# Performance work log

Measured on AMD Instinct MI355X. Metric: run time of the kernel, lower is better.

## Reference

```python
import jax, jax.numpy as jnp
import numpy as np

N_HEADS = 8
D_MODEL = 256
HEAD_DEPTH = D_MODEL // N_HEADS
B, S = 2, 4096


def setup_inputs() -> dict:
    key = jax.random.key(0)
    ks = jax.random.split(key, 8)
    scale = 1.0 / np.sqrt(D_MODEL)
    return {
        "q": jax.random.normal(ks[0], (B, S, D_MODEL), dtype=jnp.float32),
        "k": jax.random.normal(ks[1], (B, S, D_MODEL), dtype=jnp.float32),
        "v": jax.random.normal(ks[2], (B, S, D_MODEL), dtype=jnp.float32),
        "mask": jax.random.randint(ks[3], (B, S, S), 0, 2).astype(jnp.bool_),
        "wq": jax.random.normal(ks[4], (D_MODEL, D_MODEL), dtype=jnp.float32) * scale,
        "wk": jax.random.normal(ks[5], (D_MODEL, D_MODEL), dtype=jnp.float32) * scale,
        "wv": jax.random.normal(ks[6], (D_MODEL, D_MODEL), dtype=jnp.float32) * scale,
        "w_out": jax.random.normal(ks[7], (D_MODEL, D_MODEL), dtype=jnp.float32) * scale,
    }


def _split_heads(x):
    # [B, S, D] -> [B, H, S, Dh]
    b, s, _ = x.shape
    return x.reshape(b, s, N_HEADS, HEAD_DEPTH).transpose(0, 2, 1, 3)


def reference(q, k, v, mask, wq, wk, wv, w_out):
    Q = _split_heads(q @ wq)
    K = _split_heads(k @ wk)
    V = _split_heads(v @ wv)
    # [B, H, Sq, Sk]
    scores = jnp.einsum('bhqd,bhkd->bhqk', Q, K) / jnp.sqrt(
        jnp.asarray(HEAD_DEPTH, dtype=Q.dtype))
    # mask True -> -inf, broadcast over heads
    scores = jnp.where(mask[:, None, :, :], -jnp.inf, scores)
    probs = jax.nn.softmax(scores, axis=-1)
    attn = jnp.einsum('bhqk,bhkd->bhqd', probs, V)
    attn = attn.transpose(0, 2, 1, 3).reshape(q.shape[0], -1, D_MODEL)
    return attn @ w_out
```

## Files before the change

kernel.cpp:

```cpp
#include <hip/hip_runtime.h>
#include <stdint.h>

typedef __bf16 bf16;
typedef __bf16 bf16x8 __attribute__((ext_vector_type(8)));
typedef __bf16 bf16x4 __attribute__((ext_vector_type(4)));
typedef float  f32x4  __attribute__((ext_vector_type(4)));
typedef float  f32x8  __attribute__((ext_vector_type(8)));
typedef float  f32x16 __attribute__((ext_vector_type(16)));
typedef float  float4v __attribute__((ext_vector_type(4)));
typedef int    int4v   __attribute__((ext_vector_type(4)));
typedef unsigned int uint;
typedef unsigned long long ull;

#define QSCALE 0.25505003984214403f


__global__ __launch_bounds__(256) void transpose_w(
    const float* __restrict__ w0, const float* __restrict__ w1,
    const float* __restrict__ w2, const float* __restrict__ w3,
    bf16* __restrict__ WT) {
  const int wsel = blockIdx.z;
  const float* W = wsel == 0 ? w0 : wsel == 1 ? w1 : wsel == 2 ? w2 : w3;
  const int k0 = blockIdx.x * 64, n0 = blockIdx.y * 64;
  __shared__ __align__(16) bf16 t[64][72];
  const int tid = threadIdx.x;
  {
    const int kk = (tid >> 4) << 2;
    const int nn = (tid & 15) << 2;
#pragma unroll
    for (int r = 0; r < 4; ++r) {
      float4v a = *(const float4v*)(W + (size_t)(k0 + kk + r) * 256 + n0 + nn);
#pragma unroll
      for (int j = 0; j < 4; ++j) t[nn + j][kk + r] = (bf16)a[j];
    }
  }
  __syncthreads();
  {
    const int ni = tid >> 2;
    const int c  = (tid & 3) * 16;
    bf16x8 o0 = *(const bf16x8*)(&t[ni][c]);
    bf16x8 o1 = *(const bf16x8*)(&t[ni][c + 8]);
    bf16* dst = WT + (size_t)wsel * 65536 + (size_t)(n0 + ni) * 256 + k0 + c;
    *(bf16x8*)dst = o0;
    *(bf16x8*)(dst + 8) = o1;
  }
}

__global__ __launch_bounds__(256) void proj_pack(
    const float* __restrict__ xq, const float* __restrict__ xk, const float* __restrict__ xv,
    const bf16* __restrict__ WT,
    bf16* __restrict__ Qp, bf16* __restrict__ Kp, bf16* __restrict__ Vp,
    const int* __restrict__ mask, uint* __restrict__ M2) {
  __shared__ __align__(16) unsigned char smem[18432];
  const int tid = threadIdx.x;

  if (blockIdx.x >= 768) {
    uint* trans = (uint*)smem;
    const int pid = blockIdx.x - 768;
    const int bb = pid >> 8;
    const int qt = (pid >> 2) & 63, kc = pid & 3;
    const int q0 = qt * 64;
    const int w = tid >> 6, l = tid & 63;
    const int qrow = q0 + w * 16 + (l >> 2);
    const size_t rowbase = ((size_t)(bb * 4096 + qrow)) * 4096 + kc * 1024;
#pragma unroll
    for (int p = 0; p < 8; ++p) {
      const int kdw = p * 4 + (l & 3);
      const int4v* mp = (const int4v*)(mask + rowbase + kdw * 32);
      uint bits = 0;
#pragma unroll
      for (int j = 0; j < 8; ++j) {
        int4v m = mp[j];
#pragma unroll
        for (int i = 0; i < 4; ++i) bits |= (m[i] != 0 ? 1u : 0u) << (j * 4 + i);
      }
      trans[kdw * 72 + w * 16 + (l >> 2)] = bits;
    }
    __syncthreads();
    {
      const int r = tid >> 3, c = (tid & 7) * 4;
      int4v a = *(const int4v*)(trans + r * 72 + c);
      int4v d = *(const int4v*)(trans + r * 72 + c + 32);
      uint* o = M2 + ((size_t)(bb * 128 + kc * 32 + r)) * 4096 + q0;
      *(int4v*)(o + c) = a;
      *(int4v*)(o + c + 32) = d;
    }
    return;
  }

  const int z = blockIdx.x >> 8;
  const int r8 = blockIdx.x & 255;
  const int m0 = (r8 >> 1) * 64, n0 = (r8 & 1) * 128;
  const float* X = z == 0 ? xq : (z == 1 ? xk : xv);
  const bf16* wt = WT + (size_t)z * 65536;
  const int wave = tid >> 6, lane = tid & 63;
  const int nl = lane & 15, quad = lane >> 4;
  const int arow = m0 + wave * 16 + nl;
  const float* xrow = X + (size_t)arow * 256;

  f32x4 zero4 = {0.f, 0.f, 0.f, 0.f};
  f32x4 acc[8];
#pragma unroll
  for (int i = 0; i < 8; ++i) acc[i] = zero4;

  for (int ks = 0; ks < 8; ++ks) {
    float4v a0 = *(const float4v*)(xrow + ks * 32 + quad * 8);
    float4v a1 = *(const float4v*)(xrow + ks * 32 + quad * 8 + 4);
    bf16x8 af;
#pragma unroll
    for (int i = 0; i < 4; ++i) { af[i] = (bf16)a0[i]; af[4 + i] = (bf16)a1[i]; }
#pragma unroll
    for (int nf = 0; nf < 8; ++nf) {
      bf16x8 bfr = *(const bf16x8*)(wt + (size_t)(n0 + nf * 16 + nl) * 256 + ks * 32 + quad * 8);
      acc[nf] = __builtin_amdgcn_mfma_f32_16x16x32_bf16(af, bfr, acc[nf], 0, 0, 0);
    }
  }

  const int bq = m0 >> 12;
  const int s0 = m0 & 4095;
  const int posl = wave * 16 + quad * 4;

  if (z == 2) {
    bf16* tv = (bf16*)smem;
#pragma unroll
    for (int nf = 0; nf < 8; ++nf) {
      const int col = nf * 16 + nl;
      bf16x4 o;
#pragma unroll
      for (int rr = 0; rr < 4; ++rr) o[rr] = (bf16)acc[nf][rr];
      *(bf16x4*)(tv + (size_t)col * 72 + posl) = o;
    }
    __syncthreads();
    const int h2 = tid >> 6, ln = tid & 63;
    const int d = ln & 31, shalf = ln >> 5;
    const int h = (n0 >> 5) + h2;
    bf16* vb = Vp + (size_t)(bq * 8 + h) * 131072 + (size_t)(s0 >> 5) * 1024 + d * 8;
#pragma unroll
    for (int it = 0; it < 4; ++it) {
      const int blk = it >> 1, sub = (it & 1) * 2 + shalf;
      const int K0 = (sub >> 1) * 16 + (sub & 1) * 4;
      const bf16* src = tv + (size_t)(h2 * 32 + d) * 72 + blk * 32 + K0;
      bf16x4 g0 = *(const bf16x4*)(src);
      bf16x4 g1 = *(const bf16x4*)(src + 8);
      bf16x8 o;
#pragma unroll
      for (int j = 0; j < 4; ++j) { o[j] = g0[j]; o[4 + j] = g1[j]; }
      *(bf16x8*)(vb + (size_t)blk * 1024 + sub * 256) = o;
    }
  } else {
    bf16* tq = (bf16*)smem;
    const float scale = (z == 0) ? QSCALE : 1.0f;
#pragma unroll
    for (int nf = 0; nf < 8; ++nf) {
      const int col = nf * 16 + nl;
#pragma unroll
      for (int rr = 0; rr < 4; ++rr)
        tq[(size_t)(posl + rr) * 136 + col] = (bf16)(acc[nf][rr] * scale);
    }
    __syncthreads();
    bf16* Out = z == 0 ? Qp : Kp;
    const int h2 = tid >> 6, ln = tid & 63;
    const int h = (n0 >> 5) + h2;
    const int s = s0 + ln;
    bf16* ob = Out + (size_t)(bq * 8 + h) * 131072 + (size_t)(s >> 5) * 1024 + (s & 31) * 8;
#pragma unroll
    for (int sub = 0; sub < 4; ++sub) {
      bf16x8 o = *(const bf16x8*)(tq + (size_t)ln * 136 + h2 * 32 + sub * 8);
      *(bf16x8*)(ob + sub * 256) = o;
    }
  }
}

__global__ __launch_bounds__(256) void attn_kernel(
    const bf16* __restrict__ Qp, const bf16* __restrict__ Kp,
    const bf16* __restrict__ Vp, const uint* __restrict__ M2,
    bf16* __restrict__ Og) {
  const int id = blockIdx.x;
  const int xcd = id & 7, slot = id >> 3;
  const int bh = xcd * 2 + (slot >> 6);
  const int q0 = (slot & 63) * 64;
  const int b = bh >> 3, h = bh & 7;
  const int tid = threadIdx.x, w = tid >> 6, lane = tid & 63;
  const int nl = lane & 31, half = lane >> 5;

  __shared__ float Ored[4][32][66];
  __shared__ float Lsum[64][8];

  const size_t bhbase = (size_t)bh * 131072;
  const int so0 = half * 256 + nl * 8;
  const int so1 = 512 + half * 256 + nl * 8;

  bf16x8 qf[2][2];
#pragma unroll
  for (int qt = 0; qt < 2; ++qt) {
    const bf16* qb = Qp + bhbase + (size_t)((q0 >> 5) + qt) * 1024;
    qf[qt][0] = *(const bf16x8*)(qb + so0);
    qf[qt][1] = *(const bf16x8*)(qb + so1);
  }

  const bf16* Kw = Kp + bhbase + (size_t)w * 1024;
  const bf16* Vw = Vp + bhbase + (size_t)w * 1024;
  const uint* Mw = M2 + (size_t)b * 524288 + (size_t)w * 4096 + q0 + nl;

  f32x16 z16;
#pragma unroll
  for (int i = 0; i < 16; ++i) z16[i] = 0.f;
  f32x16 acc0 = z16, acc1 = z16;
  float lsum0 = 0.f, lsum1 = 0.f;

  struct Frag { bf16x8 ka0, ka1, va0, va1; uint m0, m1; };
  auto LOADF = [&](int kt) -> Frag {
    Frag f;
    const bf16* kc = Kw + (size_t)kt * 4096;
    const bf16* vc = Vw + (size_t)kt * 4096;
    f.ka0 = *(const bf16x8*)(kc + so0);
    f.ka1 = *(const bf16x8*)(kc + so1);
    f.va0 = *(const bf16x8*)(vc + so0);
    f.va1 = *(const bf16x8*)(vc + so1);
    const uint* mp = Mw + (size_t)kt * 16384;
    f.m0 = mp[0];
    f.m1 = mp[32];
    return f;
  };

  auto STEP = [&](const Frag& f) {
    const int minv0 = (int)((~f.m0) >> (4 * half));
    const int minv1 = (int)((~f.m1) >> (4 * half));
    f32x16 st0 = __builtin_amdgcn_mfma_f32_32x32x16_bf16(f.ka0, qf[0][0], z16, 0, 0, 0);
    st0 = __builtin_amdgcn_mfma_f32_32x32x16_bf16(f.ka1, qf[0][1], st0, 0, 0, 0);
    f32x16 st1 = __builtin_amdgcn_mfma_f32_32x32x16_bf16(f.ka0, qf[1][0], z16, 0, 0, 0);
    st1 = __builtin_amdgcn_mfma_f32_32x32x16_bf16(f.ka1, qf[1][1], st1, 0, 0, 0);

    f32x16 pf0, pf1;
#pragma unroll
    for (int g = 0; g < 4; ++g)
#pragma unroll
      for (int r = 0; r < 4; ++r) {
        const int i = g * 4 + r, off = r + 8 * g;
        float e0 = __builtin_amdgcn_exp2f(st0[i]);
        float e1 = __builtin_amdgcn_exp2f(st1[i]);
        const uint k0m = (uint)__builtin_amdgcn_sbfe(minv0, off, 1);
        const uint k1m = (uint)__builtin_amdgcn_sbfe(minv1, off, 1);
        e0 = __uint_as_float(__float_as_uint(e0) & k0m);
        e1 = __uint_as_float(__float_as_uint(e1) & k1m);
        lsum0 += e0; lsum1 += e1;
        pf0[i] = e0; pf1[i] = e1;
      }
    const bf16x8 pb00 = __builtin_convertvector(
        __builtin_shufflevector(pf0, pf0, 0, 1, 2, 3, 4, 5, 6, 7), bf16x8);
    const bf16x8 pb01 = __builtin_convertvector(
        __builtin_shufflevector(pf0, pf0, 8, 9, 10, 11, 12, 13, 14, 15), bf16x8);
    const bf16x8 pb10 = __builtin_convertvector(
        __builtin_shufflevector(pf1, pf1, 0, 1, 2, 3, 4, 5, 6, 7), bf16x8);
    const bf16x8 pb11 = __builtin_convertvector(
        __builtin_shufflevector(pf1, pf1, 8, 9, 10, 11, 12, 13, 14, 15), bf16x8);

    acc0 = __builtin_amdgcn_mfma_f32_32x32x16_bf16(f.va0, pb00, acc0, 0, 0, 0);
    acc0 = __builtin_amdgcn_mfma_f32_32x32x16_bf16(f.va1, pb01, acc0, 0, 0, 0);
    acc1 = __builtin_amdgcn_mfma_f32_32x32x16_bf16(f.va0, pb10, acc1, 0, 0, 0);
    acc1 = __builtin_amdgcn_mfma_f32_32x32x16_bf16(f.va1, pb11, acc1, 0, 0, 0);
  };

  Frag fa = LOADF(0), fb;
  for (int kt = 0; kt < 32; kt += 2) {
    fb = LOADF(kt + 1);
    STEP(fa);
    if (kt + 2 < 32) fa = LOADF(kt + 2);
    STEP(fb);
  }

#pragma unroll
  for (int g = 0; g < 4; ++g)
#pragma unroll
    for (int r = 0; r < 4; ++r) {
      const int d = r + 8 * g + 4 * half, i = g * 4 + r;
      Ored[w][d][nl] = acc0[i];
      Ored[w][d][32 + nl] = acc1[i];
    }
  Lsum[nl][w * 2 + half] = lsum0;
  Lsum[32 + nl][w * 2 + half] = lsum1;
  __syncthreads();
  if (tid < 64) {
    float s = 0.f;
#pragma unroll
    for (int j = 0; j < 8; ++j) s += Lsum[tid][j];
    Lsum[tid][0] = 1.0f / s;
  }
  __syncthreads();
  {
    const int q = tid >> 2, db = (tid & 3) * 8;
    const float rl = Lsum[q][0];
    bf16x8 o;
#pragma unroll
    for (int dj = 0; dj < 8; ++dj) {
      const float s = Ored[0][db + dj][q] + Ored[1][db + dj][q] +
                      Ored[2][db + dj][q] + Ored[3][db + dj][q];
      o[dj] = (bf16)(s * rl);
    }
    *(bf16x8*)(Og + ((size_t)(b * 4096 + q0 + q)) * 256 + h * 32 + db) = o;
  }
}

__global__ __launch_bounds__(256) void gemm_out(
    const bf16* __restrict__ A, const bf16* __restrict__ WTo, float* __restrict__ C) {
  const int m0 = blockIdx.x * 64, n0 = blockIdx.y * 64;
  const int tid = threadIdx.x, wave = tid >> 6, lane = tid & 63;
  const int nl = lane & 15, quad = lane >> 4;
  const int arow = m0 + wave * 16 + nl;

  f32x4 zero4 = {0.f, 0.f, 0.f, 0.f};
  f32x4 acc[4];
#pragma unroll
  for (int i = 0; i < 4; ++i) acc[i] = zero4;

  for (int ks = 0; ks < 8; ++ks) {
    bf16x8 af = *(const bf16x8*)(A + (size_t)arow * 256 + ks * 32 + quad * 8);
#pragma unroll
    for (int nf = 0; nf < 4; ++nf) {
      bf16x8 bfr = *(const bf16x8*)(WTo + (size_t)(n0 + nf * 16 + nl) * 256 + ks * 32 + quad * 8);
      acc[nf] = __builtin_amdgcn_mfma_f32_16x16x32_bf16(af, bfr, acc[nf], 0, 0, 0);
    }
  }
  const int Rbase = m0 + wave * 16 + quad * 4;
#pragma unroll
  for (int nf = 0; nf < 4; ++nf)
#pragma unroll
    for (int r = 0; r < 4; ++r)
      C[(size_t)(Rbase + r) * 256 + n0 + nf * 16 + nl] = acc[nf][r];
}

extern "C" void kernel_launch(void* const* d_in, const int* in_sizes, int n_in,
                              void* d_out, int out_size, void* d_ws, size_t ws_size,
                              hipStream_t stream) {
  const float* q  = (const float*)d_in[0];
  const float* k  = (const float*)d_in[1];
  const float* v  = (const float*)d_in[2];
  const int*  mask = (const int*)d_in[3];
  const float* wq = (const float*)d_in[4];
  const float* wk = (const float*)d_in[5];
  const float* wv = (const float*)d_in[6];
  const float* wo = (const float*)d_in[7];
  float* out = (float*)d_out;

  uint8_t* ws = (uint8_t*)d_ws;
  bf16* WT = (bf16*)ws;
  bf16* Qp = (bf16*)(ws + (512u << 10));
  bf16* Kp = Qp + 2097152;
  bf16* Vp = Kp + 2097152;
  uint* Mb = (uint*)((uint8_t*)(Vp + 2097152));
  bf16* Ao = (bf16*)((uint8_t*)Mb + (4u << 20));

  transpose_w<<<dim3(4, 4, 4), 256, 0, stream>>>(wq, wk, wv, wo, WT);
  proj_pack<<<dim3(768 + 512), 256, 0, stream>>>(q, k, v, WT, Qp, Kp, Vp, mask, Mb);
  attn_kernel<<<dim3(1024), 256, 0, stream>>>(Qp, Kp, Vp, Mb, Ao);
  gemm_out<<<dim3(128, 4), 256, 0, stream>>>(Ao, WT + 3 * 65536, out);
}
```

Before: 327.3 us.

## Pack mask bits with wave ballots, coalesced loads, and reorder blocks

The mask-packing blocks now read the int mask with fully coalesced per-lane int4 loads and build bit words via wave ballots instead of per-thread strided scans. The bit layout in the packed mask changes, so the attention kernel's bit-extract offsets are updated to match. Mask blocks are also placed before the projection blocks, and the row-sum accumulation in attention uses paired float2 adds. The aim is to cut the cost of the 128MB mask read, which dominates memory traffic, but it depends on the new bit layout matching exactly.

```diff
diff --git a/kernel.cpp b/kernel.cpp
--- a/kernel.cpp
+++ b/kernel.cpp
@@ -4,8 +4,8 @@
 typedef __bf16 bf16;
 typedef __bf16 bf16x8 __attribute__((ext_vector_type(8)));
 typedef __bf16 bf16x4 __attribute__((ext_vector_type(4)));
+typedef float  f32x2  __attribute__((ext_vector_type(2)));
 typedef float  f32x4  __attribute__((ext_vector_type(4)));
-typedef float  f32x8  __attribute__((ext_vector_type(8)));
 typedef float  f32x16 __attribute__((ext_vector_type(16)));
 typedef float  float4v __attribute__((ext_vector_type(4)));
 typedef int    int4v   __attribute__((ext_vector_type(4)));
@@ -54,42 +54,41 @@
   __shared__ __align__(16) unsigned char smem[18432];
   const int tid = threadIdx.x;
 
-  if (blockIdx.x >= 768) {
+  if (blockIdx.x < 1024) {
     uint* trans = (uint*)smem;
-    const int pid = blockIdx.x - 768;
-    const int bb = pid >> 8;
-    const int qt = (pid >> 2) & 63, kc = pid & 3;
-    const int q0 = qt * 64;
+    const int pid = blockIdx.x;
+    const int bb = pid >> 9;
+    const int qt = (pid >> 2) & 127;
+    const int kc = pid & 3;
+    const int q0 = qt * 32;
     const int w = tid >> 6, l = tid & 63;
-    const int qrow = q0 + w * 16 + (l >> 2);
-    const size_t rowbase = ((size_t)(bb * 4096 + qrow)) * 4096 + kc * 1024;
-#pragma unroll
-    for (int p = 0; p < 8; ++p) {
-      const int kdw = p * 4 + (l & 3);
-      const int4v* mp = (const int4v*)(mask + rowbase + kdw * 32);
-      uint bits = 0;
-#pragma unroll
-      for (int j = 0; j < 8; ++j) {
-        int4v m = mp[j];
-#pragma unroll
-        for (int i = 0; i < 4; ++i) bits |= (m[i] != 0 ? 1u : 0u) << (j * 4 + i);
+    const int d2 = l & 7;
+    const int sh = 8 * d2;
+#pragma unroll 4
+    for (int t = 0; t < 32; ++t) {
+      const int q_l = w * 8 + (t >> 2), c = t & 3;
+      const int4v m = *(const int4v*)(mask + ((size_t)(bb * 4096 + q0 + q_l)) * 4096 +
+                                      kc * 1024 + c * 256 + 4 * l);
+      uint out = 0;
+#pragma unroll
+      for (int i = 0; i < 4; ++i) {
+        ull b = __ballot(m[i] != 0);
+        out |= ((uint)(b >> sh) & 0xFFu) << (8 * i);
       }
-      trans[kdw * 72 + w * 16 + (l >> 2)] = bits;
+      if (l < 8) trans[(c * 8 + d2) * 36 + q_l] = out;
     }
     __syncthreads();
     {
-      const int r = tid >> 3, c = (tid & 7) * 4;
-      int4v a = *(const int4v*)(trans + r * 72 + c);
-      int4v d = *(const int4v*)(trans + r * 72 + c + 32);
-      uint* o = M2 + ((size_t)(bb * 128 + kc * 32 + r)) * 4096 + q0;
-      *(int4v*)(o + c) = a;
-      *(int4v*)(o + c + 32) = d;
+      const int r = tid >> 3, c4 = (tid & 7) * 4;
+      int4v a = *(const int4v*)(trans + r * 36 + c4);
+      *(int4v*)(M2 + ((size_t)(bb * 128 + kc * 32 + r)) * 4096 + q0 + c4) = a;
     }
     return;
   }
 
-  const int z = blockIdx.x >> 8;
-  const int r8 = blockIdx.x & 255;
+  const int pb = blockIdx.x - 1024;
+  const int z = pb >> 8;
+  const int r8 = pb & 255;
   const int m0 = (r8 >> 1) * 64, n0 = (r8 & 1) * 128;
   const float* X = z == 0 ? xq : (z == 1 ? xk : xv);
   const bf16* wt = WT + (size_t)z * 65536;
@@ -206,7 +205,7 @@
 #pragma unroll
   for (int i = 0; i < 16; ++i) z16[i] = 0.f;
   f32x16 acc0 = z16, acc1 = z16;
-  float lsum0 = 0.f, lsum1 = 0.f;
+  f32x2 ls0 = {0.f, 0.f}, ls1 = {0.f, 0.f};
 
   struct Frag { bf16x8 ka0, ka1, va0, va1; uint m0, m1; };
   auto LOADF = [&](int kt) -> Frag {
@@ -224,8 +223,8 @@
   };
 
   auto STEP = [&](const Frag& f) {
-    const int minv0 = (int)((~f.m0) >> (4 * half));
-    const int minv1 = (int)((~f.m1) >> (4 * half));
+    const int minv0 = (int)((~f.m0) >> half);
+    const int minv1 = (int)((~f.m1) >> half);
     f32x16 st0 = __builtin_amdgcn_mfma_f32_32x32x16_bf16(f.ka0, qf[0][0], z16, 0, 0, 0);
     st0 = __builtin_amdgcn_mfma_f32_32x32x16_bf16(f.ka1, qf[0][1], st0, 0, 0, 0);
     f32x16 st1 = __builtin_amdgcn_mfma_f32_32x32x16_bf16(f.ka0, qf[1][0], z16, 0, 0, 0);
@@ -236,16 +235,21 @@
     for (int g = 0; g < 4; ++g)
 #pragma unroll
       for (int r = 0; r < 4; ++r) {
-        const int i = g * 4 + r, off = r + 8 * g;
+        const int i = g * 4 + r, off = 8 * r + 2 * g;
         float e0 = __builtin_amdgcn_exp2f(st0[i]);
         float e1 = __builtin_amdgcn_exp2f(st1[i]);
         const uint k0m = (uint)__builtin_amdgcn_sbfe(minv0, off, 1);
         const uint k1m = (uint)__builtin_amdgcn_sbfe(minv1, off, 1);
         e0 = __uint_as_float(__float_as_uint(e0) & k0m);
         e1 = __uint_as_float(__float_as_uint(e1) & k1m);
-        lsum0 += e0; lsum1 += e1;
         pf0[i] = e0; pf1[i] = e1;
       }
+#pragma unroll
+    for (int i = 0; i < 16; i += 2) {
+      f32x2 a0 = {pf0[i], pf0[i + 1]};
+      f32x2 a1 = {pf1[i], pf1[i + 1]};
+      ls0 += a0; ls1 += a1;
+    }
     const bf16x8 pb00 = __builtin_convertvector(
         __builtin_shufflevector(pf0, pf0, 0, 1, 2, 3, 4, 5, 6, 7), bf16x8);
     const bf16x8 pb01 = __builtin_convertvector(
@@ -277,8 +281,8 @@
       Ored[w][d][nl] = acc0[i];
       Ored[w][d][32 + nl] = acc1[i];
     }
-  Lsum[nl][w * 2 + half] = lsum0;
-  Lsum[32 + nl][w * 2 + half] = lsum1;
+  Lsum[nl][w * 2 + half] = ls0.x + ls0.y;
+  Lsum[32 + nl][w * 2 + half] = ls1.x + ls1.y;
   __syncthreads();
   if (tid < 64) {
     float s = 0.f;
@@ -351,7 +355,7 @@
   bf16* Ao = (bf16*)((uint8_t*)Mb + (4u << 20));
 
   transpose_w<<<dim3(4, 4, 4), 256, 0, stream>>>(wq, wk, wv, wo, WT);
-  proj_pack<<<dim3(768 + 512), 256, 0, stream>>>(q, k, v, WT, Qp, Kp, Vp, mask, Mb);
+  proj_pack<<<dim3(1024 + 768), 256, 0, stream>>>(q, k, v, WT, Qp, Kp, Vp, mask, Mb);
   attn_kernel<<<dim3(1024), 256, 0, stream>>>(Qp, Kp, Vp, Mb, Ao);
   gemm_out<<<dim3(128, 4), 256, 0, stream>>>(Ao, WT + 3 * 65536, out);
 }
```

After: 336.8 us. 2.9% more time.
